# Kernel optimization log

Hardware: AMD Instinct MI355X
Metric: run time of the kernel (lower is better)

## Reference

```python
import jax, jax.numpy as jnp
import numpy as np

B, T, IN, H, L = 262144, 30, 1, 5, 5  # batch, seq_len, input_size, hidden_size, num_layers


def setup_inputs() -> dict:
    key = jax.random.key(0)
    ks = jax.random.split(key, 9)
    s = 1.0 / np.sqrt(H)  # PyTorch GRU init: U(-1/sqrt(H), 1/sqrt(H))
    u = lambda k, shape: jax.random.uniform(k, shape, jnp.float32, -s, s)
    return {
        "x": jax.random.normal(ks[0], (B, IN, T), jnp.float32),
        "w_ih0": u(ks[1], (2, 3 * H, IN)),      # layer 0, [dir, 3H, in]
        "w_hh0": u(ks[2], (2, 3 * H, H)),
        "b_ih0": u(ks[3], (2, 3 * H)),
        "b_hh0": u(ks[4], (2, 3 * H)),
        "w_ih": u(ks[5], (L - 1, 2, 3 * H, 2 * H)),  # layers 1..4 consume bidir output (2H)
        "w_hh": u(ks[6], (L - 1, 2, 3 * H, H)),
        "b_ih": u(ks[7], (L - 1, 2, 3 * H)),
        "b_hh": u(ks[8], (L - 1, 2, 3 * H)),
    }


def _gru_dir(x_seq, w_ih, w_hh, b_ih, b_hh, reverse):
    """Single-direction GRU over x_seq [B, T, D] -> outputs [B, T, H] (PyTorch gate math)."""
    def step(h, x_t):
        gi = x_t @ w_ih.T + b_ih            # [B, 3H]
        gh = h @ w_hh.T + b_hh              # [B, 3H]
        i_r, i_z, i_n = jnp.split(gi, 3, axis=-1)
        h_r, h_z, h_n = jnp.split(gh, 3, axis=-1)
        r = jax.nn.sigmoid(i_r + h_r)
        z = jax.nn.sigmoid(i_z + h_z)
        n = jnp.tanh(i_n + r * h_n)
        h_new = (1.0 - z) * n + z * h
        return h_new, h_new

    h0 = jnp.zeros((x_seq.shape[0], w_hh.shape[1]), x_seq.dtype)
    # scan over time; reverse=True matches PyTorch's reverse direction (output kept in
    # original time order, ys[t] = hidden after consuming x[T-1..t]).
    _, ys = jax.lax.scan(step, h0, jnp.swapaxes(x_seq, 0, 1), reverse=reverse)
    return jnp.swapaxes(ys, 0, 1)


def reference(x, w_ih0, w_hh0, b_ih0, b_hh0, w_ih, w_hh, b_ih, b_hh):
    h = jnp.transpose(x, (0, 2, 1))  # [B, C, T] -> [B, T, C]
    wih = [w_ih0] + [w_ih[l] for l in range(w_ih.shape[0])]
    whh = [w_hh0] + [w_hh[l] for l in range(w_hh.shape[0])]
    bih = [b_ih0] + [b_ih[l] for l in range(b_ih.shape[0])]
    bhh = [b_hh0] + [b_hh[l] for l in range(b_hh.shape[0])]
    for l in range(len(wih)):
        fwd = _gru_dir(h, wih[l][0], whh[l][0], bih[l][0], bhh[l][0], False)
        bwd = _gru_dir(h, wih[l][1], whh[l][1], bih[l][1], bhh[l][1], True)
        h = jnp.concatenate([fwd, bwd], axis=-1)  # [B, T, 2H]
    return h[:, -1:, :]  # out[:, -1, :].unsqueeze(1) -> [B, 1, 2H]
```

## Files before the change

### kernel.cpp

```cpp
#include <hip/hip_runtime.h>


#define NB 262144
#define T 30
#define NBLK (NB / 32)
#define SEQW (T * 5 * 32)

typedef _Float16 f16x8 __attribute__((ext_vector_type(8)));
typedef float f32x16 __attribute__((ext_vector_type(16)));

__device__ unsigned g_seq[(unsigned long long)NBLK * SEQW];

#define SIG_SCALE  (-1.4426950408889634f)
#define TANH_SCALE ( 2.8853900817779268f)

__device__ __forceinline__ float sig_s(float xs) {
    return __builtin_amdgcn_rcpf(1.0f + __builtin_amdgcn_exp2f(xs));
}
__device__ __forceinline__ float tanh_s(float xs) {
    return fmaf(-2.0f, __builtin_amdgcn_rcpf(1.0f + __builtin_amdgcn_exp2f(xs)), 1.0f);
}
__device__ __forceinline__ unsigned packh(_Float16 a, _Float16 b) {
    union { _Float16 f; unsigned short s; } ua, ub;
    ua.f = a; ub.f = b;
    return (unsigned)ua.s | ((unsigned)ub.s << 16);
}

template <bool IS_L0, int NT, bool WRITE, bool STORE, bool G_R, bool G_W>
__device__ __forceinline__ void run_layer(
    const float* __restrict__ wih, const float* __restrict__ whh,
    const float* __restrict__ bih, const float* __restrict__ bhh,
    const unsigned* seqR, unsigned* seqW, const float* xg,
    float* outp, const int d, const int lane)
{
    const int lr   = lane & 31;
    const int half = lane >> 5;

    const int q_r = lr >> 3;
    const int h_r = (lr >> 2) & 1;
    const int g   = lr & 3;
    const int u_r = 2 * q_r + 1 - h_r;
    const bool rv = (q_r < 3) && (u_r < 5);

    f16x8 af;
#pragma unroll
    for (int e = 0; e < 8; e++) {
        const int k = 8 * half + e;
        float v = 0.f;
        if (rv) {
            if (!IS_L0) {
                if (k < 10) {
                    const int j = (k & 1) * 5 + (k >> 1);
                    if (g == 0)      v = SIG_SCALE  * wih[u_r * 10 + j];
                    else if (g == 1) v = SIG_SCALE  * wih[(5 + u_r) * 10 + j];
                    else if (g == 2) v = TANH_SCALE * wih[(10 + u_r) * 10 + j];
                } else if (k < 15) {
                    const int uh = k - 10;
                    if (g == 0)      v = SIG_SCALE  * whh[u_r * 5 + uh];
                    else if (g == 1) v = SIG_SCALE  * whh[(5 + u_r) * 5 + uh];
                    else if (g == 3) v = TANH_SCALE * whh[(10 + u_r) * 5 + uh];
                }
            } else {
                if (k == 0) {
                    if (g == 0)      v = SIG_SCALE  * wih[u_r];
                    else if (g == 1) v = SIG_SCALE  * wih[5 + u_r];
                    else if (g == 2) v = TANH_SCALE * wih[10 + u_r];
                } else if (k >= 10 && k < 15) {
                    const int uh = k - 10;
                    if (g == 0)      v = SIG_SCALE  * whh[u_r * 5 + uh];
                    else if (g == 1) v = SIG_SCALE  * whh[(5 + u_r) * 5 + uh];
                    else if (g == 3) v = TANH_SCALE * whh[(10 + u_r) * 5 + uh];
                }
            }
        }
        af[e] = (_Float16)v;
    }

    f32x16 bc;
#pragma unroll
    for (int q = 0; q < 4; q++) {
        const int u = 2 * q + 1 - half;
        float b0 = 0.f, b1 = 0.f, b2 = 0.f, b3 = 0.f;
        if (q < 3 && u < 5) {
            b0 = SIG_SCALE  * (bih[u] + bhh[u]);
            b1 = SIG_SCALE  * (bih[5 + u] + bhh[5 + u]);
            b2 = TANH_SCALE * bih[10 + u];
            b3 = TANH_SCALE * bhh[10 + u];
        }
        bc[4 * q + 0] = b0; bc[4 * q + 1] = b1;
        bc[4 * q + 2] = b2; bc[4 * q + 3] = b3;
    }

    const int sdir = d ? -1 : 1;
    const int p0   = d ? (T - 1) : 0;
    const unsigned* rbase = seqR + p0 * 160 + lr;
    const int r0off = half ? 128 : 0;
    _Float16* wbase = (_Float16*)seqW + p0 * 320 + lr * 2 + d;
    const int rstep = sdir * 160, wstep = sdir * 320;
    const int paddr = (lane ^ 32) << 2;

    float h0 = 0.f, h1 = 0.f, h2 = 0.f;
    unsigned pb1 = 0, pb2 = 0, pb3 = 0;

    auto step = [&](unsigned B0, unsigned B1, unsigned B2, unsigned B3) {
        union { f16x8 v; unsigned u[4]; } B;
        B.u[0] = B0;
        B.u[1] = half ? pb1 : B1;
        B.u[2] = half ? pb2 : B2;
        B.u[3] = half ? pb3 : B3;

        const f32x16 D = __builtin_amdgcn_mfma_f32_32x32x16_f16(af, B.v, bc, 0, 0, 0);

        float r, z, n;
        r = sig_s(D[0]); z = sig_s(D[1]);
        n = tanh_s(fmaf(r, D[3], D[2]));
        h0 = fmaf(z, h0 - n, n);
        r = sig_s(D[4]); z = sig_s(D[5]);
        n = tanh_s(fmaf(r, D[7], D[6]));
        h1 = fmaf(z, h1 - n, n);

        const _Float16 q0f = (_Float16)h0, q1f = (_Float16)h1;
        const unsigned pks = packh(q0f, q1f);
        const unsigned o = (unsigned)__builtin_amdgcn_ds_bpermute(paddr, (int)pks);

        r = sig_s(D[8]); z = sig_s(D[9]);
        n = tanh_s(fmaf(r, D[11], D[10]));
        h2 = fmaf(z, h2 - n, n);
        const _Float16 q2f = (_Float16)h2;

        pb1 = __builtin_amdgcn_perm(pks, o, 0x01000504u);
        pb2 = __builtin_amdgcn_perm(pks, o, 0x03020706u);
        pb3 = packh(q2f, (_Float16)0.f);

        if constexpr (WRITE) {
            wbase[(1 - half) * 64] = q0f;
            wbase[(3 - half) * 64] = q1f;
            if (half) wbase[4 * 64] = q2f;
            wbase += wstep;
        }
    };

    if constexpr (IS_L0) {
        const float* xp = xg + lr * T + p0;
        float xf = *xp;
        for (int s = 0; s < NT; s++) {
            const unsigned xv = packh((_Float16)xf, (_Float16)0.f);
            if (s + 1 < NT) { xp += sdir; xf = *xp; }
            step(half ? 0u : xv, 0u, 0u, 0u);
        }
    } else if constexpr (!G_R) {
        const unsigned* rb = rbase;
        unsigned c0 = rb[r0off], c1 = rb[32], c2 = rb[64], c3 = rb[96];
        for (int s = 0; s < NT; s++) {
            const unsigned t0 = c0, t1 = c1, t2 = c2, t3 = c3;
            if (s + 1 < NT) {
                rb += rstep;
                c0 = rb[r0off]; c1 = rb[32]; c2 = rb[64]; c3 = rb[96];
            }
            step(t0, t1, t2, t3);
        }
    } else if constexpr (NT == 1) {
        const unsigned a0 = rbase[r0off], a1 = rbase[32],
                       a2 = rbase[64],   a3 = rbase[96];
        step(a0, a1, a2, a3);
    } else {
        const unsigned* rn = rbase;
        unsigned a0 = rn[r0off], a1 = rn[32], a2 = rn[64], a3 = rn[96];
        rn += rstep;
        unsigned b0 = rn[r0off], b1 = rn[32], b2 = rn[64], b3 = rn[96];
        rn += rstep;
        for (int s = 0; s < NT; s += 2) {
            step(a0, a1, a2, a3);
            if (s + 2 < NT) {
                a0 = rn[r0off]; a1 = rn[32]; a2 = rn[64]; a3 = rn[96];
                rn += rstep;
            }
            step(b0, b1, b2, b3);
            if (s + 3 < NT) {
                b0 = rn[r0off]; b1 = rn[32]; b2 = rn[64]; b3 = rn[96];
                rn += rstep;
            }
        }
    }

    if constexpr (STORE) {
        outp[1 - half] = h0;
        outp[3 - half] = h1;
        if (half) outp[4] = h2;
    }
}

__global__ void __launch_bounds__(128, 4) gru_all(
    const float* __restrict__ x,
    const float* __restrict__ wih0, const float* __restrict__ whh0,
    const float* __restrict__ bih0, const float* __restrict__ bhh0,
    const float* __restrict__ wihL, const float* __restrict__ whhL,
    const float* __restrict__ bihL, const float* __restrict__ bhhL,
    float* __restrict__ out)
{
    __shared__ unsigned S[T][5][32];

    const int tid  = threadIdx.x;
    const int d    = tid >> 6;
    const int lane = tid & 63;
    const int lr   = lane & 31;
    const long base = (long)blockIdx.x * 32;

    const float* xg = x + base * T;
    unsigned* G = g_seq + (unsigned long long)blockIdx.x * SEQW;

    run_layer<true, T, true, false, false, false>(
        wih0 + d * 15, whh0 + d * 75, bih0 + d * 15, bhh0 + d * 15,
        nullptr, &S[0][0][0], xg, nullptr, d, lane);
    __syncthreads();

    run_layer<false, T, true, false, false, true>(
        wihL + (0 + d) * 150, whhL + (0 + d) * 75, bihL + (0 + d) * 15, bhhL + (0 + d) * 15,
        &S[0][0][0], G, nullptr, nullptr, d, lane);
    __syncthreads();

    run_layer<false, T, true, false, true, false>(
        wihL + (2 + d) * 150, whhL + (2 + d) * 75, bihL + (2 + d) * 15, bhhL + (2 + d) * 15,
        G, &S[0][0][0], nullptr, nullptr, d, lane);
    __syncthreads();

    run_layer<false, T, true, false, false, true>(
        wihL + (4 + d) * 150, whhL + (4 + d) * 75, bihL + (4 + d) * 15, bhhL + (4 + d) * 15,
        &S[0][0][0], G, nullptr, nullptr, d, lane);
    __syncthreads();

    {
        float* op = out + (base + lr) * 10 + d * 5;
        if (d == 0)
            run_layer<false, T, false, true, true, false>(
                wihL + 6 * 150, whhL + 6 * 75, bihL + 6 * 15, bhhL + 6 * 15,
                G, nullptr, nullptr, op, d, lane);
        else
            run_layer<false, 1, false, true, true, false>(
                wihL + 7 * 150, whhL + 7 * 75, bihL + 7 * 15, bhhL + 7 * 15,
                G, nullptr, nullptr, op, d, lane);
    }
}

extern "C" void kernel_launch(void* const* d_in, const int* in_sizes, int n_in,
                              void* d_out, int out_size, void* d_ws, size_t ws_size,
                              hipStream_t stream) {
    const float* x    = (const float*)d_in[0];
    const float* wih0 = (const float*)d_in[1];
    const float* whh0 = (const float*)d_in[2];
    const float* bih0 = (const float*)d_in[3];
    const float* bhh0 = (const float*)d_in[4];
    const float* wihL = (const float*)d_in[5];
    const float* whhL = (const float*)d_in[6];
    const float* bihL = (const float*)d_in[7];
    const float* bhhL = (const float*)d_in[8];
    float* out = (float*)d_out;

    gru_all<<<NBLK, 128, 0, stream>>>(x, wih0, whh0, bih0, bhh0,
                                      wihL, whhL, bihL, bhhL, out);
}
```

Before: 448.8 us.

## Replace LDS sequence buffer with global ping-pong buffers and raise occupancy hint

Removes the shared-memory sequence buffer and instead ping-pongs the inter-layer sequence between two per-block global scratch regions, so every layer reads and writes through global memory (mostly L2-resident). This frees LDS and, together with raising launch_bounds min-blocks from 4 to 8, is meant to allow more resident blocks per CU to hide recurrence latency. The trade-off is more global traffic and higher load latency on layers that used to read from LDS, plus twice the scratch footprint.

```diff
diff --git a/kernel.cpp b/kernel.cpp
--- a/kernel.cpp
+++ b/kernel.cpp
@@ -9,7 +9,7 @@
 typedef _Float16 f16x8 __attribute__((ext_vector_type(8)));
 typedef float f32x16 __attribute__((ext_vector_type(16)));
 
-__device__ unsigned g_seq[(unsigned long long)NBLK * SEQW];
+__device__ unsigned g_seq[(unsigned long long)NBLK * 2 * SEQW];
 
 #define SIG_SCALE  (-1.4426950408889634f)
 #define TANH_SCALE ( 2.8853900817779268f)
@@ -26,7 +26,7 @@
     return (unsigned)ua.s | ((unsigned)ub.s << 16);
 }
 
-template <bool IS_L0, int NT, bool WRITE, bool STORE, bool G_R, bool G_W>
+template <bool IS_L0, int NT, bool WRITE, bool STORE>
 __device__ __forceinline__ void run_layer(
     const float* __restrict__ wih, const float* __restrict__ whh,
     const float* __restrict__ bih, const float* __restrict__ bhh,
@@ -148,17 +148,6 @@
             if (s + 1 < NT) { xp += sdir; xf = *xp; }
             step(half ? 0u : xv, 0u, 0u, 0u);
         }
-    } else if constexpr (!G_R) {
-        const unsigned* rb = rbase;
-        unsigned c0 = rb[r0off], c1 = rb[32], c2 = rb[64], c3 = rb[96];
-        for (int s = 0; s < NT; s++) {
-            const unsigned t0 = c0, t1 = c1, t2 = c2, t3 = c3;
-            if (s + 1 < NT) {
-                rb += rstep;
-                c0 = rb[r0off]; c1 = rb[32]; c2 = rb[64]; c3 = rb[96];
-            }
-            step(t0, t1, t2, t3);
-        }
     } else if constexpr (NT == 1) {
         const unsigned a0 = rbase[r0off], a1 = rbase[32],
                        a2 = rbase[64],   a3 = rbase[96];
@@ -190,7 +179,7 @@
     }
 }
 
-__global__ void __launch_bounds__(128, 4) gru_all(
+__global__ void __launch_bounds__(128, 8) gru_all(
     const float* __restrict__ x,
     const float* __restrict__ wih0, const float* __restrict__ whh0,
     const float* __restrict__ bih0, const float* __restrict__ bhh0,
@@ -198,8 +187,6 @@
     const float* __restrict__ bihL, const float* __restrict__ bhhL,
     float* __restrict__ out)
 {
-    __shared__ unsigned S[T][5][32];
-
     const int tid  = threadIdx.x;
     const int d    = tid >> 6;
     const int lane = tid & 63;
@@ -207,38 +194,39 @@
     const long base = (long)blockIdx.x * 32;
 
     const float* xg = x + base * T;
-    unsigned* G = g_seq + (unsigned long long)blockIdx.x * SEQW;
-
-    run_layer<true, T, true, false, false, false>(
+    unsigned* G0 = g_seq + (unsigned long long)blockIdx.x * (2 * SEQW);
+    unsigned* G1 = G0 + SEQW;
+
+    run_layer<true, T, true, false>(
         wih0 + d * 15, whh0 + d * 75, bih0 + d * 15, bhh0 + d * 15,
-        nullptr, &S[0][0][0], xg, nullptr, d, lane);
-    __syncthreads();
-
-    run_layer<false, T, true, false, false, true>(
+        nullptr, G0, xg, nullptr, d, lane);
+    __syncthreads();
+
+    run_layer<false, T, true, false>(
         wihL + (0 + d) * 150, whhL + (0 + d) * 75, bihL + (0 + d) * 15, bhhL + (0 + d) * 15,
-        &S[0][0][0], G, nullptr, nullptr, d, lane);
-    __syncthreads();
-
-    run_layer<false, T, true, false, true, false>(
+        G0, G1, nullptr, nullptr, d, lane);
+    __syncthreads();
+
+    run_layer<false, T, true, false>(
         wihL + (2 + d) * 150, whhL + (2 + d) * 75, bihL + (2 + d) * 15, bhhL + (2 + d) * 15,
-        G, &S[0][0][0], nullptr, nullptr, d, lane);
-    __syncthreads();
-
-    run_layer<false, T, true, false, false, true>(
+        G1, G0, nullptr, nullptr, d, lane);
+    __syncthreads();
+
+    run_layer<false, T, true, false>(
         wihL + (4 + d) * 150, whhL + (4 + d) * 75, bihL + (4 + d) * 15, bhhL + (4 + d) * 15,
-        &S[0][0][0], G, nullptr, nullptr, d, lane);
+        G0, G1, nullptr, nullptr, d, lane);
     __syncthreads();
 
     {
         float* op = out + (base + lr) * 10 + d * 5;
         if (d == 0)
-            run_layer<false, T, false, true, true, false>(
+            run_layer<false, T, false, true>(
                 wihL + 6 * 150, whhL + 6 * 75, bihL + 6 * 15, bhhL + 6 * 15,
-                G, nullptr, nullptr, op, d, lane);
+                G1, nullptr, nullptr, op, d, lane);
         else
-            run_layer<false, 1, false, true, true, false>(
+            run_layer<false, 1, false, true>(
                 wihL + 7 * 150, whhL + 7 * 75, bihL + 7 * 15, bhhL + 7 * 15,
-                G, nullptr, nullptr, op, d, lane);
+                G1, nullptr, nullptr, op, d, lane);
     }
 }
 
```

After: 1.211 ms. +169.9%, slower.

## Remap MFMA K layout so recurrent hidden state stays lane-local, dropping bpermute

Applied to the files above, without the earlier changes.

Reorders the MFMA A-operand K dimension and the hidden-unit-to-lane mapping so each half-wave's own hidden outputs land directly in the B-operand slots it needs. This removes the per-step ds_bpermute cross-half exchange from the serial recurrence, replacing it with byte perms. Sequence reads drop from four to three words per step, and the unused G_W template parameter is removed. The risk is a subtle mismatch in the weight/bias index remapping across halves, which would produce wrong results.

```diff
diff --git a/kernel.cpp b/kernel.cpp
--- a/kernel.cpp
+++ b/kernel.cpp
@@ -20,13 +20,15 @@
 __device__ __forceinline__ float tanh_s(float xs) {
     return fmaf(-2.0f, __builtin_amdgcn_rcpf(1.0f + __builtin_amdgcn_exp2f(xs)), 1.0f);
 }
+__device__ __forceinline__ unsigned hbits(_Float16 a) {
+    union { _Float16 f; unsigned short s; } u; u.f = a;
+    return (unsigned)u.s;
+}
 __device__ __forceinline__ unsigned packh(_Float16 a, _Float16 b) {
-    union { _Float16 f; unsigned short s; } ua, ub;
-    ua.f = a; ub.f = b;
-    return (unsigned)ua.s | ((unsigned)ub.s << 16);
-}
-
-template <bool IS_L0, int NT, bool WRITE, bool STORE, bool G_R, bool G_W>
+    return hbits(a) | (hbits(b) << 16);
+}
+
+template <bool IS_L0, int NT, bool WRITE, bool STORE, bool G_R>
 __device__ __forceinline__ void run_layer(
     const float* __restrict__ wih, const float* __restrict__ whh,
     const float* __restrict__ bih, const float* __restrict__ bhh,
@@ -36,11 +38,9 @@
     const int lr   = lane & 31;
     const int half = lane >> 5;
 
-    const int q_r = lr >> 3;
-    const int h_r = (lr >> 2) & 1;
+    const int u_r = lr >> 2;
     const int g   = lr & 3;
-    const int u_r = 2 * q_r + 1 - h_r;
-    const bool rv = (q_r < 3) && (u_r < 5);
+    const bool rv = lr < 20;
 
     f16x8 af;
 #pragma unroll
@@ -49,13 +49,19 @@
         float v = 0.f;
         if (rv) {
             if (!IS_L0) {
-                if (k < 10) {
-                    const int j = (k & 1) * 5 + (k >> 1);
+                if (k <= 4 || (k >= 8 && k <= 12)) {
+                    const int idx = (k < 8) ? k : (k - 3);
+                    const int j = (idx & 1) * 5 + (idx >> 1);
                     if (g == 0)      v = SIG_SCALE  * wih[u_r * 10 + j];
                     else if (g == 1) v = SIG_SCALE  * wih[(5 + u_r) * 10 + j];
                     else if (g == 2) v = TANH_SCALE * wih[(10 + u_r) * 10 + j];
-                } else if (k < 15) {
-                    const int uh = k - 10;
+                } else if (k >= 5 && k <= 7) {
+                    const int uh = 2 * (k - 5);
+                    if (g == 0)      v = SIG_SCALE  * whh[u_r * 5 + uh];
+                    else if (g == 1) v = SIG_SCALE  * whh[(5 + u_r) * 5 + uh];
+                    else if (g == 3) v = TANH_SCALE * whh[(10 + u_r) * 5 + uh];
+                } else if (k == 13 || k == 14) {
+                    const int uh = 2 * (k - 13) + 1;
                     if (g == 0)      v = SIG_SCALE  * whh[u_r * 5 + uh];
                     else if (g == 1) v = SIG_SCALE  * whh[(5 + u_r) * 5 + uh];
                     else if (g == 3) v = TANH_SCALE * whh[(10 + u_r) * 5 + uh];
@@ -65,8 +71,13 @@
                     if (g == 0)      v = SIG_SCALE  * wih[u_r];
                     else if (g == 1) v = SIG_SCALE  * wih[5 + u_r];
                     else if (g == 2) v = TANH_SCALE * wih[10 + u_r];
-                } else if (k >= 10 && k < 15) {
-                    const int uh = k - 10;
+                } else if (k >= 5 && k <= 7) {
+                    const int uh = 2 * (k - 5);
+                    if (g == 0)      v = SIG_SCALE  * whh[u_r * 5 + uh];
+                    else if (g == 1) v = SIG_SCALE  * whh[(5 + u_r) * 5 + uh];
+                    else if (g == 3) v = TANH_SCALE * whh[(10 + u_r) * 5 + uh];
+                } else if (k == 13 || k == 14) {
+                    const int uh = 2 * (k - 13) + 1;
                     if (g == 0)      v = SIG_SCALE  * whh[u_r * 5 + uh];
                     else if (g == 1) v = SIG_SCALE  * whh[(5 + u_r) * 5 + uh];
                     else if (g == 3) v = TANH_SCALE * whh[(10 + u_r) * 5 + uh];
@@ -79,7 +90,7 @@
     f32x16 bc;
 #pragma unroll
     for (int q = 0; q < 4; q++) {
-        const int u = 2 * q + 1 - half;
+        const int u = 2 * q + half;
         float b0 = 0.f, b1 = 0.f, b2 = 0.f, b3 = 0.f;
         if (q < 3 && u < 5) {
             b0 = SIG_SCALE  * (bih[u] + bhh[u]);
@@ -91,23 +102,30 @@
         bc[4 * q + 2] = b2; bc[4 * q + 3] = b3;
     }
 
+    const unsigned S01 = half ? 0x05040302u : 0x03020100u;
+    const unsigned S2  = half ? 0x05040302u : 0x05040100u;
+
     const int sdir = d ? -1 : 1;
     const int p0   = d ? (T - 1) : 0;
-    const unsigned* rbase = seqR + p0 * 160 + lr;
-    const int r0off = half ? 128 : 0;
+    const unsigned* rbase = seqR + p0 * 160 + lr + (half ? 64 : 0);
     _Float16* wbase = (_Float16*)seqW + p0 * 320 + lr * 2 + d;
     const int rstep = sdir * 160, wstep = sdir * 320;
-    const int paddr = (lane ^ 32) << 2;
 
     float h0 = 0.f, h1 = 0.f, h2 = 0.f;
-    unsigned pb1 = 0, pb2 = 0, pb3 = 0;
-
-    auto step = [&](unsigned B0, unsigned B1, unsigned B2, unsigned B3) {
+    unsigned hw2 = 0, hw3 = 0;
+
+    auto step = [&](unsigned pa, unsigned pb, unsigned pc, unsigned xv) {
         union { f16x8 v; unsigned u[4]; } B;
-        B.u[0] = B0;
-        B.u[1] = half ? pb1 : B1;
-        B.u[2] = half ? pb2 : B2;
-        B.u[3] = half ? pb3 : B3;
+        if constexpr (!IS_L0) {
+            B.u[0] = __builtin_amdgcn_perm(pb, pa, S01);
+            B.u[1] = __builtin_amdgcn_perm(pc, pb, S01);
+            B.u[2] = __builtin_amdgcn_perm(hw2, pc, S2);
+        } else {
+            B.u[0] = half ? 0u : xv;
+            B.u[1] = 0u;
+            B.u[2] = hw2 << 16;
+        }
+        B.u[3] = hw3;
 
         const f32x16 D = __builtin_amdgcn_mfma_f32_32x32x16_f16(af, B.v, bc, 0, 0, 0);
 
@@ -118,24 +136,18 @@
         r = sig_s(D[4]); z = sig_s(D[5]);
         n = tanh_s(fmaf(r, D[7], D[6]));
         h1 = fmaf(z, h1 - n, n);
-
-        const _Float16 q0f = (_Float16)h0, q1f = (_Float16)h1;
-        const unsigned pks = packh(q0f, q1f);
-        const unsigned o = (unsigned)__builtin_amdgcn_ds_bpermute(paddr, (int)pks);
-
         r = sig_s(D[8]); z = sig_s(D[9]);
         n = tanh_s(fmaf(r, D[11], D[10]));
         h2 = fmaf(z, h2 - n, n);
-        const _Float16 q2f = (_Float16)h2;
-
-        pb1 = __builtin_amdgcn_perm(pks, o, 0x01000504u);
-        pb2 = __builtin_amdgcn_perm(pks, o, 0x03020706u);
-        pb3 = packh(q2f, (_Float16)0.f);
+
+        const _Float16 q0f = (_Float16)h0, q1f = (_Float16)h1, q2f = (_Float16)h2;
+        hw2 = hbits(q0f);
+        hw3 = packh(q1f, q2f);
 
         if constexpr (WRITE) {
-            wbase[(1 - half) * 64] = q0f;
-            wbase[(3 - half) * 64] = q1f;
-            if (half) wbase[4 * 64] = q2f;
+            wbase[half * 64]       = q0f;
+            wbase[(2 + half) * 64] = q1f;
+            if (!half) wbase[4 * 64] = q2f;
             wbase += wstep;
         }
     };
@@ -144,49 +156,47 @@
         const float* xp = xg + lr * T + p0;
         float xf = *xp;
         for (int s = 0; s < NT; s++) {
-            const unsigned xv = packh((_Float16)xf, (_Float16)0.f);
+            const unsigned xv = hbits((_Float16)xf);
             if (s + 1 < NT) { xp += sdir; xf = *xp; }
-            step(half ? 0u : xv, 0u, 0u, 0u);
+            step(0u, 0u, 0u, xv);
         }
     } else if constexpr (!G_R) {
         const unsigned* rb = rbase;
-        unsigned c0 = rb[r0off], c1 = rb[32], c2 = rb[64], c3 = rb[96];
+        unsigned a0 = rb[0], a1 = rb[32], a2 = rb[64];
         for (int s = 0; s < NT; s++) {
-            const unsigned t0 = c0, t1 = c1, t2 = c2, t3 = c3;
+            const unsigned t0 = a0, t1 = a1, t2 = a2;
             if (s + 1 < NT) {
                 rb += rstep;
-                c0 = rb[r0off]; c1 = rb[32]; c2 = rb[64]; c3 = rb[96];
-            }
-            step(t0, t1, t2, t3);
+                a0 = rb[0]; a1 = rb[32]; a2 = rb[64];
+            }
+            step(t0, t1, t2, 0u);
         }
     } else if constexpr (NT == 1) {
-        const unsigned a0 = rbase[r0off], a1 = rbase[32],
-                       a2 = rbase[64],   a3 = rbase[96];
-        step(a0, a1, a2, a3);
+        step(rbase[0], rbase[32], rbase[64], 0u);
     } else {
         const unsigned* rn = rbase;
-        unsigned a0 = rn[r0off], a1 = rn[32], a2 = rn[64], a3 = rn[96];
+        unsigned a0 = rn[0], a1 = rn[32], a2 = rn[64];
         rn += rstep;
-        unsigned b0 = rn[r0off], b1 = rn[32], b2 = rn[64], b3 = rn[96];
+        unsigned b0 = rn[0], b1 = rn[32], b2 = rn[64];
         rn += rstep;
         for (int s = 0; s < NT; s += 2) {
-            step(a0, a1, a2, a3);
+            step(a0, a1, a2, 0u);
             if (s + 2 < NT) {
-                a0 = rn[r0off]; a1 = rn[32]; a2 = rn[64]; a3 = rn[96];
+                a0 = rn[0]; a1 = rn[32]; a2 = rn[64];
                 rn += rstep;
             }
-            step(b0, b1, b2, b3);
+            step(b0, b1, b2, 0u);
             if (s + 3 < NT) {
-                b0 = rn[r0off]; b1 = rn[32]; b2 = rn[64]; b3 = rn[96];
+                b0 = rn[0]; b1 = rn[32]; b2 = rn[64];
                 rn += rstep;
             }
         }
     }
 
     if constexpr (STORE) {
-        outp[1 - half] = h0;
-        outp[3 - half] = h1;
-        if (half) outp[4] = h2;
+        outp[half]     = h0;
+        outp[2 + half] = h1;
+        if (!half) outp[4] = h2;
     }
 }
 
@@ -209,22 +219,22 @@
     const float* xg = x + base * T;
     unsigned* G = g_seq + (unsigned long long)blockIdx.x * SEQW;
 
-    run_layer<true, T, true, false, false, false>(
+    run_layer<true, T, true, false, false>(
         wih0 + d * 15, whh0 + d * 75, bih0 + d * 15, bhh0 + d * 15,
         nullptr, &S[0][0][0], xg, nullptr, d, lane);
     __syncthreads();
 
-    run_layer<false, T, true, false, false, true>(
+    run_layer<false, T, true, false, false>(
         wihL + (0 + d) * 150, whhL + (0 + d) * 75, bihL + (0 + d) * 15, bhhL + (0 + d) * 15,
         &S[0][0][0], G, nullptr, nullptr, d, lane);
     __syncthreads();
 
-    run_layer<false, T, true, false, true, false>(
+    run_layer<false, T, true, false, true>(
         wihL + (2 + d) * 150, whhL + (2 + d) * 75, bihL + (2 + d) * 15, bhhL + (2 + d) * 15,
         G, &S[0][0][0], nullptr, nullptr, d, lane);
     __syncthreads();
 
-    run_layer<false, T, true, false, false, true>(
+    run_layer<false, T, true, false, false>(
         wihL + (4 + d) * 150, whhL + (4 + d) * 75, bihL + (4 + d) * 15, bhhL + (4 + d) * 15,
         &S[0][0][0], G, nullptr, nullptr, d, lane);
     __syncthreads();
@@ -232,11 +242,11 @@
     {
         float* op = out + (base + lr) * 10 + d * 5;
         if (d == 0)
-            run_layer<false, T, false, true, true, false>(
+            run_layer<false, T, false, true, true>(
                 wihL + 6 * 150, whhL + 6 * 75, bihL + 6 * 15, bhhL + 6 * 15,
                 G, nullptr, nullptr, op, d, lane);
         else
-            run_layer<false, 1, false, true, true, false>(
+            run_layer<false, 1, false, true, true>(
                 wihL + 7 * 150, whhL + 7 * 75, bihL + 7 * 15, bhhL + 7 * 15,
                 G, nullptr, nullptr, op, d, lane);
     }
```

After: 437.3 us. -2.6%, faster.
